# Optimization experiments

Hardware: AMD Instinct MI355X
Metric: run time of the kernel (lower is better)

The kernel has to match this reference:

```python
import jax, jax.numpy as jnp
import numpy as np

N = 50000      # graph nodes
E = 800000     # edges
R = 8          # relations
D = 128        # entity_dim == relation_dim == n_hidden
L = 2          # gnn layers
NE = 150000    # entity vocab
NEG_SLOPE = 0.01


def setup_inputs() -> dict:
    key = jax.random.key(0)
    ks = jax.random.split(key, 9)
    return {
        "node_ids": jax.random.randint(ks[0], (N,), 0, NE),
        "relation_ids": jax.random.randint(ks[1], (E,), 0, R),
        "src": jax.random.randint(ks[2], (E,), 0, N),
        "dst": jax.random.randint(ks[3], (E,), 0, N),
        "entity_table": jax.random.normal(ks[4], (NE, D), dtype=jnp.float32) * 0.1,
        "relation_table": jax.random.normal(ks[5], (R, D), dtype=jnp.float32) * 0.1,
        "relation_W": jax.random.normal(ks[6], (R, D, D), dtype=jnp.float32) * 0.1,
        "res_fc_W": jax.random.normal(ks[7], (L, D, D), dtype=jnp.float32) * 0.1,
        "res_fc2_W": jax.random.normal(ks[8], (L, D, D), dtype=jnp.float32) * 0.1,
    }


def _kgat_layer(h, efeat, rel, src, dst, relation_W, W1, W2):
    # project every node by every relation weight: (N, R, D)
    proj = jnp.einsum('nd,rde->nre', h, relation_W)
    t_r = proj[src, rel]            # (E, D)  W_r h_src
    h_r = proj[dst, rel]            # (E, D)  W_r h_dst
    # att = (W_r h_t)^T tanh(W_r h_dst + e_r)
    att = jnp.sum(t_r * jnp.tanh(h_r + efeat), axis=1)  # (E,)
    # edge softmax over incoming edges of each dst node
    m = jax.ops.segment_max(att, dst, num_segments=N)
    ex = jnp.exp(att - m[dst])
    s = jax.ops.segment_sum(ex, dst, num_segments=N)
    a = ex / s[dst]                 # (E,)
    # message = a * h_src, scatter-sum to dst
    h_nb = jax.ops.segment_sum(h[src] * a[:, None], dst, num_segments=N)  # (N, D)
    out = (jax.nn.leaky_relu((h + h_nb) @ W1.T, NEG_SLOPE)
           + jax.nn.leaky_relu((h * h_nb) @ W2.T, NEG_SLOPE))
    return h_nb, out


def reference(node_ids, relation_ids, src, dst, entity_table, relation_table,
              relation_W, res_fc_W, res_fc2_W):
    h = entity_table[node_ids]           # (N, D)
    efeat = relation_table[relation_ids]  # (E, D)
    cache = [h]
    for i in range(L):
        h, out = _kgat_layer(h, efeat, relation_ids, src, dst,
                             relation_W, res_fc_W[i], res_fc2_W[i])
        cache.append(out)
    return jnp.concatenate(cache, axis=1)  # (N, D*(L+1))
```

## Files before the change

### kernel.cpp

```cpp
#include <hip/hip_runtime.h>
#include <math.h>

#define DDIM 128
#define RREL 8

typedef _Float16 f16;
typedef __attribute__((ext_vector_type(2))) _Float16 h2;
typedef __attribute__((ext_vector_type(8))) _Float16 f16x8;
typedef __attribute__((ext_vector_type(4))) float f32x4;

static __device__ __forceinline__ unsigned short f2h(float f) {
    union { _Float16 h; unsigned short s; } c; c.h = (_Float16)f; return c.s;
}
static __device__ __forceinline__ h2 u2h(unsigned u) {
    union { unsigned u; h2 h; } c; c.u = u; return c.h;
}
static __device__ __forceinline__ unsigned h2u(h2 h) {
    union { unsigned u; h2 h; } c; c.h = h; return c.u;
}
static __device__ __forceinline__ float lrelu(float x) {
    return x > 0.0f ? x : 0.01f * x;
}
static __device__ __forceinline__ float tanh_fast(float x) {
    float e = __expf(2.0f * x);
    return 1.0f - 2.0f * __builtin_amdgcn_rcpf(e + 1.0f);
}

__global__ __launch_bounds__(256) void prep_weights(const float* __restrict__ relW,
                                                    const float* __restrict__ fcW,
                                                    const float* __restrict__ fc2W,
                                                    unsigned short* __restrict__ Wt,
                                                    unsigned short* __restrict__ Wq,
                                                    unsigned short* __restrict__ Wb1,
                                                    unsigned short* __restrict__ Wb2) {
    int i = blockIdx.x * 256 + threadIdx.x;
    const int NT = RREL * DDIM * DDIM;
    const int NF = 2 * DDIM * DDIM;
    if (i < NT) {
        float w = relW[i];
        int r = i >> 14;
        int d = (i >> 7) & 127;
        int e = i & 127;
        unsigned short h = f2h(w);
        Wt[(r << 14) + (e << 7) + d] = h;
        Wq[i] = h;
    } else if (i < NT + NF) {
        int j = i - NT;
        Wb1[j] = f2h(fcW[j]);
    } else if (i < NT + 2 * NF) {
        int j = i - NT - NF;
        Wb2[j] = f2h(fc2W[j]);
    }
}

__global__ __launch_bounds__(256) void gather_h0(const int* __restrict__ node_ids,
                                                 const float* __restrict__ etab,
                                                 unsigned short* __restrict__ hb0,
                                                 float* __restrict__ out, int N) {
    int i = blockIdx.x * 256 + threadIdx.x;
    if (i >= N * 32) return;
    int n = i >> 5;
    int c4 = (i & 31) * 4;
    float4 v = *(const float4*)(etab + (size_t)node_ids[n] * DDIM + c4);
    *(float4*)(out + (size_t)n * 384 + c4) = v;
    unsigned lo = (unsigned)f2h(v.x) | ((unsigned)f2h(v.y) << 16);
    unsigned hi = (unsigned)f2h(v.z) | ((unsigned)f2h(v.w) << 16);
    *(uint2*)(hb0 + (size_t)n * DDIM + c4) = make_uint2(lo, hi);
}

__global__ __launch_bounds__(256) void hist_k(const int* __restrict__ dst,
                                              int* __restrict__ counts, int E) {
    int i = blockIdx.x * 256 + threadIdx.x;
    if (i < E) atomicAdd(counts + dst[i], 1);
}

__global__ __launch_bounds__(256) void scan_a(const int* __restrict__ counts,
                                              int* __restrict__ tmp,
                                              int* __restrict__ part, int N) {
    __shared__ int sh[256];
    int i = blockIdx.x * 256 + threadIdx.x;
    int v = (i < N) ? counts[i] : 0;
    sh[threadIdx.x] = v;
    __syncthreads();
    #pragma unroll
    for (int o = 1; o < 256; o <<= 1) {
        int t = (threadIdx.x >= o) ? sh[threadIdx.x - o] : 0;
        __syncthreads();
        sh[threadIdx.x] += t;
        __syncthreads();
    }
    if (i < N) tmp[i] = sh[threadIdx.x];
    if (threadIdx.x == 255) part[blockIdx.x] = sh[255];
}

__global__ __launch_bounds__(256) void scan_b(int* __restrict__ part, int nb) {
    __shared__ int sh[256];
    int v = (threadIdx.x < nb) ? part[threadIdx.x] : 0;
    sh[threadIdx.x] = v;
    __syncthreads();
    #pragma unroll
    for (int o = 1; o < 256; o <<= 1) {
        int t = (threadIdx.x >= o) ? sh[threadIdx.x - o] : 0;
        __syncthreads();
        sh[threadIdx.x] += t;
        __syncthreads();
    }
    if (threadIdx.x < nb) part[threadIdx.x] = sh[threadIdx.x] - v;
}

__global__ __launch_bounds__(256) void scan_c(const int* __restrict__ counts,
                                              const int* __restrict__ tmp,
                                              const int* __restrict__ part,
                                              int* __restrict__ row_ptr,
                                              int* __restrict__ woff, int N) {
    int i = blockIdx.x * 256 + threadIdx.x;
    if (i >= N) return;
    int incl = tmp[i] + part[blockIdx.x];
    row_ptr[i + 1] = incl;
    woff[i] = incl - counts[i];
    if (i == 0) row_ptr[0] = 0;
}

__global__ __launch_bounds__(256) void scatter_k(const int* __restrict__ src,
                                                 const int* __restrict__ rel,
                                                 const int* __restrict__ dst,
                                                 int* __restrict__ woff,
                                                 int2* __restrict__ epack, int E) {
    int i = blockIdx.x * 256 + threadIdx.x;
    if (i >= E) return;
    int p = atomicAdd(woff + dst[i], 1);
    epack[p] = make_int2(src[i], rel[i]);
}

__global__ __launch_bounds__(256, 3) void prq_gemm(const unsigned short* __restrict__ hb,
                                                   const unsigned short* __restrict__ Wt,
                                                   const unsigned short* __restrict__ Wq,
                                                   const float* __restrict__ rtab,
                                                   unsigned short* __restrict__ qout, int N) {
    __shared__ __align__(16) unsigned short As[128][136];
    int tid = threadIdx.x;
    int row0 = blockIdx.x * 128;
    int r = blockIdx.y;

    #pragma unroll
    for (int j = 0; j < 8; ++j) {
        int idx = j * 256 + tid;
        int row = idx >> 4;
        int c8 = (idx & 15) * 8;
        int grow = row0 + row;
        uint4 v = make_uint4(0, 0, 0, 0);
        if (grow < N) v = *(const uint4*)(hb + (size_t)grow * DDIM + c8);
        *(uint4*)(&As[row][c8]) = v;
    }
    __syncthreads();

    int wave = tid >> 6, lane = tid & 63;
    int wr = wave >> 1, wc = wave & 1;
    int m = lane & 15, quad = lane >> 4;

    const unsigned short* WtR = Wt + (r << 14);
    const unsigned short* WqR = Wq + (r << 14);

    f32x4 acc[4][4];
    #pragma unroll
    for (int mt = 0; mt < 4; ++mt)
        #pragma unroll
        for (int nt = 0; nt < 4; ++nt) acc[mt][nt] = (f32x4){0.f, 0.f, 0.f, 0.f};

    #pragma unroll
    for (int kk = 0; kk < 4; ++kk) {
        f16x8 af[4], bfr[4];
        #pragma unroll
        for (int i = 0; i < 4; ++i)
            bfr[i] = *(const f16x8*)(WtR + (((wc * 64 + i * 16 + m)) << 7) + kk * 32 + quad * 8);
        #pragma unroll
        for (int i = 0; i < 4; ++i)
            af[i] = *(const f16x8*)(&As[wr * 64 + i * 16 + m][kk * 32 + quad * 8]);
        #pragma unroll
        for (int mt = 0; mt < 4; ++mt)
            #pragma unroll
            for (int nt = 0; nt < 4; ++nt)
                acc[mt][nt] = __builtin_amdgcn_mfma_f32_16x16x32_f16(af[mt], bfr[nt], acc[mt][nt], 0, 0, 0);
    }
    __syncthreads();

    float rv[4];
    #pragma unroll
    for (int nt = 0; nt < 4; ++nt)
        rv[nt] = rtab[r * DDIM + wc * 64 + nt * 16 + m];
    #pragma unroll
    for (int mt = 0; mt < 4; ++mt) {
        #pragma unroll
        for (int nt = 0; nt < 4; ++nt) {
            #pragma unroll
            for (int q = 0; q < 4; ++q) {
                int row = wr * 64 + mt * 16 + quad * 4 + q;
                int col = wc * 64 + nt * 16 + m;
                As[row][col] = f2h(tanh_fast(acc[mt][nt][q] + rv[nt]));
            }
        }
    }
    __syncthreads();

    #pragma unroll
    for (int mt = 0; mt < 4; ++mt)
        #pragma unroll
        for (int nt = 0; nt < 4; ++nt) acc[mt][nt] = (f32x4){0.f, 0.f, 0.f, 0.f};

    #pragma unroll
    for (int kk = 0; kk < 4; ++kk) {
        f16x8 af[4], bfr[4];
        #pragma unroll
        for (int i = 0; i < 4; ++i)
            bfr[i] = *(const f16x8*)(WqR + (((wc * 64 + i * 16 + m)) << 7) + kk * 32 + quad * 8);
        #pragma unroll
        for (int i = 0; i < 4; ++i)
            af[i] = *(const f16x8*)(&As[wr * 64 + i * 16 + m][kk * 32 + quad * 8]);
        #pragma unroll
        for (int mt = 0; mt < 4; ++mt)
            #pragma unroll
            for (int nt = 0; nt < 4; ++nt)
                acc[mt][nt] = __builtin_amdgcn_mfma_f32_16x16x32_f16(af[mt], bfr[nt], acc[mt][nt], 0, 0, 0);
    }

    #pragma unroll
    for (int mt = 0; mt < 4; ++mt) {
        #pragma unroll
        for (int nt = 0; nt < 4; ++nt) {
            #pragma unroll
            for (int q = 0; q < 4; ++q) {
                int row = row0 + wr * 64 + mt * 16 + quad * 4 + q;
                int col = wc * 64 + nt * 16 + m;
                if (row < N)
                    qout[(size_t)row * 1024 + (r << 7) + col] = f2h(acc[mt][nt][q]);
            }
        }
    }
}

__global__ __launch_bounds__(256) void fused_agg(const unsigned short* __restrict__ qt,
                                                 const unsigned short* __restrict__ hb,
                                                 const int* __restrict__ row_ptr,
                                                 const int2* __restrict__ epack,
                                                 unsigned short* __restrict__ hbn, int N) {
    __shared__ __align__(16) unsigned q2[4][RREL][68];
    int wv = threadIdx.x >> 6, lane = threadIdx.x & 63;
    int n = blockIdx.x * 4 + wv;
    if (n >= N) return;
    int g  = lane >> 3;
    int gp = lane & 7;
    int dbase = gp * 16;

    #pragma unroll
    for (int r = 0; r < RREL; ++r)
        q2[wv][r][lane] = *(const unsigned*)(qt + (size_t)n * 1024 + r * 128 + lane * 2);

    int beg = row_ptr[n], end = row_ptr[n + 1];
    float s = 0.f;
    h2 a[8];
    #pragma unroll
    for (int i = 0; i < 8; ++i) a[i] = u2h(0u);

    for (int base = beg; base < end; base += 8) {
        int eidx = base + g;
        bool act = eidx < end;
        int2 ep = act ? epack[eidx] : make_int2(0, 0);
        int sr = ep.x, rr = ep.y;
        const unsigned short* hp = hb + (size_t)sr * DDIM + dbase;
        uint4 hv0 = *(const uint4*)(hp);
        uint4 hv1 = *(const uint4*)(hp + 8);
        const unsigned* tp = &q2[wv][rr][gp * 8];
        uint4 t0 = *(const uint4*)(tp);
        uint4 t1 = *(const uint4*)(tp + 4);

        h2 vs = u2h(hv0.x) * u2h(t0.x);
        vs += u2h(hv0.y) * u2h(t0.y);
        vs += u2h(hv0.z) * u2h(t0.z);
        vs += u2h(hv0.w) * u2h(t0.w);
        vs += u2h(hv1.x) * u2h(t1.x);
        vs += u2h(hv1.y) * u2h(t1.y);
        vs += u2h(hv1.z) * u2h(t1.z);
        vs += u2h(hv1.w) * u2h(t1.w);
        float v = (float)vs.x + (float)vs.y;
        v += __shfl_xor(v, 1, 64);
        v += __shfl_xor(v, 2, 64);
        v += __shfl_xor(v, 4, 64);

        float p = act ? __expf(fminf(v, 10.f)) : 0.f;
        s += p;
        h2 ph;
        ph.x = (_Float16)p;
        ph.y = ph.x;
        a[0] += ph * u2h(hv0.x);
        a[1] += ph * u2h(hv0.y);
        a[2] += ph * u2h(hv0.z);
        a[3] += ph * u2h(hv0.w);
        a[4] += ph * u2h(hv1.x);
        a[5] += ph * u2h(hv1.y);
        a[6] += ph * u2h(hv1.z);
        a[7] += ph * u2h(hv1.w);
    }

    #pragma unroll
    for (int st = 8; st < 64; st <<= 1) {
        s += __shfl_xor(s, st, 64);
        #pragma unroll
        for (int i = 0; i < 8; ++i) {
            unsigned t = (unsigned)__shfl_xor((int)h2u(a[i]), st, 64);
            a[i] += u2h(t);
        }
    }

    float inv = (end > beg) ? 1.0f / s : 0.0f;

    if (g == 0) {
        unsigned pk[8];
        #pragma unroll
        for (int i = 0; i < 8; ++i) {
            float lo = (float)a[i].x * inv;
            float hi = (float)a[i].y * inv;
            h2 o;
            o.x = (_Float16)lo;
            o.y = (_Float16)hi;
            pk[i] = h2u(o);
        }
        unsigned short* bp = hbn + (size_t)n * DDIM + gp * 16;
        *(uint4*)(bp)     = make_uint4(pk[0], pk[1], pk[2], pk[3]);
        *(uint4*)(bp + 8) = make_uint4(pk[4], pk[5], pk[6], pk[7]);
    }
}

__global__ __launch_bounds__(256) void out_gemm(const unsigned short* __restrict__ hb,
                                                const unsigned short* __restrict__ hbn,
                                                const unsigned short* __restrict__ W1,
                                                const unsigned short* __restrict__ W2,
                                                float* __restrict__ out,
                                                int colbase, int N) {
    __shared__ __align__(16) unsigned short As[64][136];
    __shared__ __align__(16) unsigned short Bs[128][136];
    int tid = threadIdx.x;
    int row0 = blockIdx.x * 64;
    int wave = tid >> 6, lane = tid & 63;
    int m = lane & 15, quad = lane >> 4;

    f32x4 acc[2][8];
    #pragma unroll
    for (int p = 0; p < 2; ++p)
        #pragma unroll
        for (int t = 0; t < 8; ++t) acc[p][t] = (f32x4){0.f, 0.f, 0.f, 0.f};

    #pragma unroll
    for (int p = 0; p < 2; ++p) {
        #pragma unroll
        for (int j = 0; j < 4; ++j) {
            int idx = j * 256 + tid;
            int row = idx >> 4;
            int c8 = (idx & 15) * 8;
            int grow = row0 + row;
            unsigned pk[4] = {0, 0, 0, 0};
            if (grow < N) {
                uint4 hv = *(const uint4*)(hb + (size_t)grow * DDIM + c8);
                uint4 nv = *(const uint4*)(hbn + (size_t)grow * DDIM + c8);
                unsigned hw[4] = {hv.x, hv.y, hv.z, hv.w};
                unsigned nw[4] = {nv.x, nv.y, nv.z, nv.w};
                #pragma unroll
                for (int jj = 0; jj < 4; ++jj) {
                    h2 hh = u2h(hw[jj]), nn = u2h(nw[jj]);
                    h2 r = p ? (h2)(hh * nn) : (h2)(hh + nn);
                    pk[jj] = h2u(r);
                }
            }
            *(uint4*)(&As[row][c8]) = make_uint4(pk[0], pk[1], pk[2], pk[3]);
        }
        const unsigned short* W = p ? W2 : W1;
        #pragma unroll
        for (int j = 0; j < 8; ++j) {
            int idx = j * 256 + tid;
            int brow = idx >> 4;
            int c8 = (idx & 15) * 8;
            *(uint4*)(&Bs[brow][c8]) = *(const uint4*)(W + ((size_t)brow << 7) + c8);
        }
        __syncthreads();

        #pragma unroll
        for (int kk = 0; kk < 4; ++kk) {
            f16x8 av = *(const f16x8*)(&As[wave * 16 + m][kk * 32 + quad * 8]);
            #pragma unroll
            for (int t = 0; t < 8; ++t) {
                f16x8 b = *(const f16x8*)(&Bs[t * 16 + m][kk * 32 + quad * 8]);
                acc[p][t] = __builtin_amdgcn_mfma_f32_16x16x32_f16(av, b, acc[p][t], 0, 0, 0);
            }
        }
        __syncthreads();
    }

    #pragma unroll
    for (int t = 0; t < 8; ++t) {
        #pragma unroll
        for (int q = 0; q < 4; ++q) {
            int row = row0 + wave * 16 + quad * 4 + q;
            int col = t * 16 + m;
            if (row < N)
                out[(size_t)row * 384 + colbase + col] =
                    lrelu(acc[0][t][q]) + lrelu(acc[1][t][q]);
        }
    }
}

extern "C" void kernel_launch(void* const* d_in, const int* in_sizes, int n_in,
                              void* d_out, int out_size, void* d_ws, size_t ws_size,
                              hipStream_t stream) {
    const int* node_ids = (const int*)d_in[0];
    const int* rel_ids  = (const int*)d_in[1];
    const int* src      = (const int*)d_in[2];
    const int* dst      = (const int*)d_in[3];
    const float* etab   = (const float*)d_in[4];
    const float* rtab   = (const float*)d_in[5];
    const float* relW   = (const float*)d_in[6];
    const float* fcW    = (const float*)d_in[7];
    const float* fc2W   = (const float*)d_in[8];
    float* out = (float*)d_out;

    const int N = in_sizes[0];
    const int E = in_sizes[1];
    const int NB = (N + 255) / 256;

    char* ws = (char*)d_ws;
    size_t off = 0;
    auto alloc = [&](size_t bytes) -> char* {
        char* p = ws + off;
        off = (off + bytes + 255) & ~(size_t)255;
        return p;
    };
    unsigned short* hb[3];
    hb[0] = (unsigned short*)alloc((size_t)N * DDIM * 2);
    hb[1] = (unsigned short*)alloc((size_t)N * DDIM * 2);
    hb[2] = (unsigned short*)alloc((size_t)N * DDIM * 2);
    unsigned short* Wt  = (unsigned short*)alloc((size_t)RREL * DDIM * DDIM * 2);
    unsigned short* Wq  = (unsigned short*)alloc((size_t)RREL * DDIM * DDIM * 2);
    unsigned short* Wb1 = (unsigned short*)alloc((size_t)2 * DDIM * DDIM * 2);
    unsigned short* Wb2 = (unsigned short*)alloc((size_t)2 * DDIM * DDIM * 2);
    unsigned short* qt  = (unsigned short*)alloc((size_t)N * RREL * DDIM * 2);
    int*  counts  = (int*)alloc((size_t)N * 4);
    int*  tmp     = (int*)alloc((size_t)N * 4);
    int*  part    = (int*)alloc((size_t)NB * 4);
    int*  row_ptr = (int*)alloc((size_t)(N + 1) * 4);
    int*  woff    = (int*)alloc((size_t)N * 4);
    int2* epack   = (int2*)alloc((size_t)E * 8);

    const int NW = RREL * DDIM * DDIM + 4 * DDIM * DDIM;
    hipLaunchKernelGGL(prep_weights, dim3((NW + 255) / 256), dim3(256), 0, stream,
                       relW, fcW, fc2W, Wt, Wq, Wb1, Wb2);
    hipLaunchKernelGGL(gather_h0, dim3((N * 32 + 255) / 256), dim3(256), 0, stream,
                       node_ids, etab, hb[0], out, N);

    hipMemsetAsync(counts, 0, (size_t)N * 4, stream);
    hipLaunchKernelGGL(hist_k, dim3((E + 255) / 256), dim3(256), 0, stream, dst, counts, E);
    hipLaunchKernelGGL(scan_a, dim3(NB), dim3(256), 0, stream, counts, tmp, part, N);
    hipLaunchKernelGGL(scan_b, dim3(1), dim3(256), 0, stream, part, NB);
    hipLaunchKernelGGL(scan_c, dim3(NB), dim3(256), 0, stream, counts, tmp, part, row_ptr, woff, N);
    hipLaunchKernelGGL(scatter_k, dim3((E + 255) / 256), dim3(256), 0, stream,
                       src, rel_ids, dst, woff, epack, E);

    for (int l = 0; l < 2; ++l) {
        hipLaunchKernelGGL(prq_gemm, dim3((N + 127) / 128, 8), dim3(256), 0, stream,
                           hb[l], Wt, Wq, rtab, qt, N);
        hipLaunchKernelGGL(fused_agg, dim3((N + 3) / 4), dim3(256), 0, stream,
                           qt, hb[l], row_ptr, epack, hb[l + 1], N);
        hipLaunchKernelGGL(out_gemm, dim3((N + 63) / 64), dim3(256), 0, stream,
                           hb[l], hb[l + 1], Wb1 + (size_t)l * DDIM * DDIM, Wb2 + (size_t)l * DDIM * DDIM,
                           out, (l + 1) * DDIM, N);
    }
}
```

Baseline: 512.7 us.

## Stage prq_gemm output through LDS for coalesced stores, load A directly

The relation-projection GEMM now stages its fp16 output tile through shared memory and writes it back as 16-byte row-contiguous chunks, replacing scattered 2-byte stores into the large per-relation output. The A operand is read straight from global memory into MFMA fragments instead of being staged through LDS first. The Wq fragments are prefetched into registers before the tanh epilogue. The occupancy hint is dropped from the launch bounds. The extra registers for the prefetched weights may lower occupancy, and the unguarded direct A loads can read past the last valid row when N is not a multiple of 128.

```diff
diff --git a/kernel.cpp b/kernel.cpp
--- a/kernel.cpp
+++ b/kernel.cpp
@@ -132,15 +132,103 @@
     epack[p] = make_int2(src[i], rel[i]);
 }
 
-__global__ __launch_bounds__(256, 3) void prq_gemm(const unsigned short* __restrict__ hb,
-                                                   const unsigned short* __restrict__ Wt,
-                                                   const unsigned short* __restrict__ Wq,
-                                                   const float* __restrict__ rtab,
-                                                   unsigned short* __restrict__ qout, int N) {
-    __shared__ __align__(16) unsigned short As[128][136];
+__global__ __launch_bounds__(256) void prq_gemm(const unsigned short* __restrict__ hb,
+                                                const unsigned short* __restrict__ Wt,
+                                                const unsigned short* __restrict__ Wq,
+                                                const float* __restrict__ rtab,
+                                                unsigned short* __restrict__ qout, int N) {
+    __shared__ __align__(16) unsigned short Ts[128][136];
     int tid = threadIdx.x;
     int row0 = blockIdx.x * 128;
     int r = blockIdx.y;
+
+    int wave = tid >> 6, lane = tid & 63;
+    int wr = wave >> 1, wc = wave & 1;
+    int m = lane & 15, quad = lane >> 4;
+
+    const unsigned short* WtR = Wt + (r << 14);
+    const unsigned short* WqR = Wq + (r << 14);
+    const unsigned short* hbase = hb + (size_t)(row0 + wr * 64 + m) * DDIM;
+
+    f32x4 acc[4][4];
+    #pragma unroll
+    for (int mt = 0; mt < 4; ++mt)
+        #pragma unroll
+        for (int nt = 0; nt < 4; ++nt) acc[mt][nt] = (f32x4){0.f, 0.f, 0.f, 0.f};
+
+    #pragma unroll
+    for (int kk = 0; kk < 4; ++kk) {
+        f16x8 af[4], bfr[4];
+        #pragma unroll
+        for (int i = 0; i < 4; ++i)
+            bfr[i] = *(const f16x8*)(WtR + ((wc * 64 + i * 16 + m) << 7) + kk * 32 + quad * 8);
+        #pragma unroll
+        for (int i = 0; i < 4; ++i)
+            af[i] = *(const f16x8*)(hbase + (size_t)(i * 16) * DDIM + kk * 32 + quad * 8);
+        #pragma unroll
+        for (int mt = 0; mt < 4; ++mt)
+            #pragma unroll
+            for (int nt = 0; nt < 4; ++nt)
+                acc[mt][nt] = __builtin_amdgcn_mfma_f32_16x16x32_f16(af[mt], bfr[nt], acc[mt][nt], 0, 0, 0);
+    }
+
+    f16x8 bq[4][4];
+    #pragma unroll
+    for (int kk = 0; kk < 4; ++kk)
+        #pragma unroll
+        for (int i = 0; i < 4; ++i)
+            bq[kk][i] = *(const f16x8*)(WqR + ((wc * 64 + i * 16 + m) << 7) + kk * 32 + quad * 8);
+
+    float rv[4];
+    #pragma unroll
+    for (int nt = 0; nt < 4; ++nt)
+        rv[nt] = rtab[r * DDIM + wc * 64 + nt * 16 + m];
+    #pragma unroll
+    for (int mt = 0; mt < 4; ++mt) {
+        #pragma unroll
+        for (int nt = 0; nt < 4; ++nt) {
+            #pragma unroll
+            for (int q = 0; q < 4; ++q) {
+                int row = wr * 64 + mt * 16 + quad * 4 + q;
+                int col = wc * 64 + nt * 16 + m;
+                Ts[row][col] = f2h(tanh_fast(acc[mt][nt][q] + rv[nt]));
+            }
+        }
+    }
+    __syncthreads();
+
+    #pragma unroll
+    for (int mt = 0; mt < 4; ++mt)
+        #pragma unroll
+        for (int nt = 0; nt < 4; ++nt) acc[mt][nt] = (f32x4){0.f, 0.f, 0.f, 0.f};
+
+    #pragma unroll
+    for (int kk = 0; kk < 4; ++kk) {
+        f16x8 af[4];
+        #pragma unroll
+        for (int i = 0; i < 4; ++i)
+            af[i] = *(const f16x8*)(&Ts[wr * 64 + i * 16 + m][kk * 32 + quad * 8]);
+        #pragma unroll
+        for (int mt = 0; mt < 4; ++mt)
+            #pragma unroll
+            for (int nt = 0; nt < 4; ++nt)
+                acc[mt][nt] = __builtin_amdgcn_mfma_f32_16x16x32_f16(af[mt], bq[kk][nt], acc[mt][nt], 0, 0, 0);
+    }
+    __syncthreads();
+
+    #pragma unroll
+    for (int mt = 0; mt < 4; ++mt) {
+        #pragma unroll
+        for (int nt = 0; nt < 4; ++nt) {
+            #pragma unroll
+            for (int q = 0; q < 4; ++q) {
+                int row = wr * 64 + mt * 16 + quad * 4 + q;
+                int col = wc * 64 + nt * 16 + m;
+                Ts[row][col] = f2h(acc[mt][nt][q]);
+            }
+        }
+    }
+    __syncthreads();
 
     #pragma unroll
     for (int j = 0; j < 8; ++j) {
@@ -148,93 +236,8 @@
         int row = idx >> 4;
         int c8 = (idx & 15) * 8;
         int grow = row0 + row;
-        uint4 v = make_uint4(0, 0, 0, 0);
-        if (grow < N) v = *(const uint4*)(hb + (size_t)grow * DDIM + c8);
-        *(uint4*)(&As[row][c8]) = v;
-    }
-    __syncthreads();
-
-    int wave = tid >> 6, lane = tid & 63;
-    int wr = wave >> 1, wc = wave & 1;
-    int m = lane & 15, quad = lane >> 4;
-
-    const unsigned short* WtR = Wt + (r << 14);
-    const unsigned short* WqR = Wq + (r << 14);
-
-    f32x4 acc[4][4];
-    #pragma unroll
-    for (int mt = 0; mt < 4; ++mt)
-        #pragma unroll
-        for (int nt = 0; nt < 4; ++nt) acc[mt][nt] = (f32x4){0.f, 0.f, 0.f, 0.f};
-
-    #pragma unroll
-    for (int kk = 0; kk < 4; ++kk) {
-        f16x8 af[4], bfr[4];
-        #pragma unroll
-        for (int i = 0; i < 4; ++i)
-            bfr[i] = *(const f16x8*)(WtR + (((wc * 64 + i * 16 + m)) << 7) + kk * 32 + quad * 8);
-        #pragma unroll
-        for (int i = 0; i < 4; ++i)
-            af[i] = *(const f16x8*)(&As[wr * 64 + i * 16 + m][kk * 32 + quad * 8]);
-        #pragma unroll
-        for (int mt = 0; mt < 4; ++mt)
-            #pragma unroll
-            for (int nt = 0; nt < 4; ++nt)
-                acc[mt][nt] = __builtin_amdgcn_mfma_f32_16x16x32_f16(af[mt], bfr[nt], acc[mt][nt], 0, 0, 0);
-    }
-    __syncthreads();
-
-    float rv[4];
-    #pragma unroll
-    for (int nt = 0; nt < 4; ++nt)
-        rv[nt] = rtab[r * DDIM + wc * 64 + nt * 16 + m];
-    #pragma unroll
-    for (int mt = 0; mt < 4; ++mt) {
-        #pragma unroll
-        for (int nt = 0; nt < 4; ++nt) {
-            #pragma unroll
-            for (int q = 0; q < 4; ++q) {
-                int row = wr * 64 + mt * 16 + quad * 4 + q;
-                int col = wc * 64 + nt * 16 + m;
-                As[row][col] = f2h(tanh_fast(acc[mt][nt][q] + rv[nt]));
-            }
-        }
-    }
-    __syncthreads();
-
-    #pragma unroll
-    for (int mt = 0; mt < 4; ++mt)
-        #pragma unroll
-        for (int nt = 0; nt < 4; ++nt) acc[mt][nt] = (f32x4){0.f, 0.f, 0.f, 0.f};
-
-    #pragma unroll
-    for (int kk = 0; kk < 4; ++kk) {
-        f16x8 af[4], bfr[4];
-        #pragma unroll
-        for (int i = 0; i < 4; ++i)
-            bfr[i] = *(const f16x8*)(WqR + (((wc * 64 + i * 16 + m)) << 7) + kk * 32 + quad * 8);
-        #pragma unroll
-        for (int i = 0; i < 4; ++i)
-            af[i] = *(const f16x8*)(&As[wr * 64 + i * 16 + m][kk * 32 + quad * 8]);
-        #pragma unroll
-        for (int mt = 0; mt < 4; ++mt)
-            #pragma unroll
-            for (int nt = 0; nt < 4; ++nt)
-                acc[mt][nt] = __builtin_amdgcn_mfma_f32_16x16x32_f16(af[mt], bfr[nt], acc[mt][nt], 0, 0, 0);
-    }
-
-    #pragma unroll
-    for (int mt = 0; mt < 4; ++mt) {
-        #pragma unroll
-        for (int nt = 0; nt < 4; ++nt) {
-            #pragma unroll
-            for (int q = 0; q < 4; ++q) {
-                int row = row0 + wr * 64 + mt * 16 + quad * 4 + q;
-                int col = wc * 64 + nt * 16 + m;
-                if (row < N)
-                    qout[(size_t)row * 1024 + (r << 7) + col] = f2h(acc[mt][nt][q]);
-            }
-        }
+        if (grow < N)
+            *(uint4*)(qout + (size_t)grow * 1024 + (r << 7) + c8) = *(const uint4*)(&Ts[row][c8]);
     }
 }
 
```

Measured after the change: 524.1 us. +2.2%, slower.
